# Kernel tuning notes

Hardware: AMD Instinct MI355X
Metric: run time of the kernel (lower is better)

## Reference

```python
import jax, jax.numpy as jnp
import numpy as np

B, T, DIM = 2, 2048, 1024
N_HEADS, HEAD_DIM, WINDOW = 16, 64, 512
EPS = 0.01


def _rmsnorm(x, gamma, eps):
    # x: [B, T, H*D] float32; normalize over last dim
    rms = jnp.sqrt(jnp.mean(jnp.square(x), axis=-1, keepdims=True) + eps)
    return x / rms * gamma


def setup_inputs() -> dict:
    key = jax.random.key(0)
    ks = jax.random.split(key, 5)
    s = 1.0 / np.sqrt(DIM)
    return {
        "x": jax.random.normal(ks[0], (B, T, DIM), jnp.float32),
        "wq": jax.random.normal(ks[1], (N_HEADS * HEAD_DIM, DIM), jnp.float32) * s,
        "wk": jax.random.normal(ks[2], (N_HEADS * HEAD_DIM, DIM), jnp.float32) * s,
        "wv": jax.random.normal(ks[3], (N_HEADS * HEAD_DIM, DIM), jnp.float32) * s,
        "wo": jax.random.normal(ks[4], (DIM, N_HEADS * HEAD_DIM), jnp.float32) * s,
        "q_gamma": jnp.ones((N_HEADS * HEAD_DIM,), jnp.float32),
        "k_gamma": jnp.ones((N_HEADS * HEAD_DIM,), jnp.float32),
    }


def reference(x, wq, wk, wv, wo, q_gamma, k_gamma):
    Bx, Tx, _ = x.shape
    H, D = N_HEADS, HEAD_DIM
    # projections (Linear with weight [out,in]): [B,T,H*D]
    q = x @ wq.T
    k = x @ wk.T
    v = (x @ wv.T).reshape(Bx, Tx, H, D).transpose(0, 2, 1, 3)  # [B,H,T,D]
    # QK RMSNorm over the flattened H*D dimension (float32 math)
    q = _rmsnorm(q, q_gamma, 1e-6).reshape(Bx, Tx, H, D).transpose(0, 2, 1, 3)
    k = _rmsnorm(k, k_gamma, 1e-6).reshape(Bx, Tx, H, D).transpose(0, 2, 1, 3)
    scale = 1.0 / np.sqrt(D)
    scores = jnp.einsum("bhqd,bhkd->bhqk", q, k) * scale  # [B,H,T,T]
    # ALiBi bias: slopes[h] * (j - i)
    slopes = jnp.asarray([2.0 ** (-8.0 / H * (h + 1)) for h in range(H)], jnp.float32)
    pos = jnp.arange(Tx)
    dist = (pos[None, :] - pos[:, None]).astype(jnp.float32)  # [T,T], dist[i,j]=j-i
    scores = scores + slopes[None, :, None, None] * dist[None, None]
    # causal (j>i) OR beyond sliding window (i-j > window_size)
    j_minus_i = pos[None, :] - pos[:, None]
    mask = (j_minus_i > 0) | (j_minus_i < -WINDOW)
    scores = jnp.where(mask[None, None], -1e9, scores)
    attn = jax.nn.softmax(scores, axis=-1)
    out = jnp.einsum("bhqk,bhkd->bhqd", attn, v)  # [B,H,T,D]
    out = out.transpose(0, 2, 1, 3).reshape(Bx, Tx, H * D)
    return out @ wo.T
```

## Files before the change

kernel.cpp:

```cpp
#include <hip/hip_runtime.h>
#include <stdint.h>

typedef unsigned short u16;
typedef __bf16 bf16x8 __attribute__((ext_vector_type(8)));
typedef float f32x4 __attribute__((ext_vector_type(4)));

#define MFMA16(a, b, c) __builtin_amdgcn_mfma_f32_16x16x32_bf16((a), (b), (c), 0, 0, 0)

__device__ __forceinline__ u16 f2bf(float f) {
  union { float f; uint32_t u; } v; v.f = f;
  uint32_t r = v.u + 0x7fffu + ((v.u >> 16) & 1u);
  return (u16)(r >> 16);
}
__device__ __forceinline__ float bf2f(u16 h) {
  union { uint32_t u; float f; } v; v.u = ((uint32_t)h) << 16;
  return v.f;
}
__device__ __forceinline__ void gload_lds16(const void* g, void* l) {
  __builtin_amdgcn_global_load_lds(
      (const __attribute__((address_space(1))) uint32_t*)(uintptr_t)g,
      (__attribute__((address_space(3))) uint32_t*)(uintptr_t)l, 16, 0, 0);
}
__device__ __forceinline__ uint32_t cvt_pk_bf16(float a, float b) {
  uint32_t r;
  asm("v_cvt_pk_bf16_f32 %0, %1, %2" : "=v"(r) : "v"(a), "v"(b));
  return r;
}

__global__ void k_cvt_all(const float* __restrict__ x, const float* __restrict__ wq,
                          const float* __restrict__ wk, const float* __restrict__ wv,
                          const float* __restrict__ wo, u16* __restrict__ xb,
                          u16* __restrict__ wqb, u16* __restrict__ wkb, u16* __restrict__ wvb,
                          u16* __restrict__ wob) {
  const int i = blockIdx.x * 256 + threadIdx.x;
  const float* src; u16* dst; int off;
  if (i < 1048576)      { src = x;  dst = xb;  off = i; }
  else if (i < 1310720) { src = wq; dst = wqb; off = i - 1048576; }
  else if (i < 1572864) { src = wk; dst = wkb; off = i - 1310720; }
  else if (i < 1835008) { src = wv; dst = wvb; off = i - 1572864; }
  else                  { src = wo; dst = wob; off = i - 1835008; }
  const float4 v = ((const float4*)src)[off];
  u16 o[4] = { f2bf(v.x), f2bf(v.y), f2bf(v.z), f2bf(v.w) };
  *(uint2*)(dst + 4 * (size_t)off) = *(const uint2*)o;
}

template <bool BF16_OUT>
__device__ __forceinline__ void gemm_core(const u16* __restrict__ A, const u16* __restrict__ Bw,
                                          void* __restrict__ C) {
  constexpr int K = 1024, N = 1024;
  __shared__ __align__(16) u16 As[128 * 32];
  __shared__ __align__(16) u16 Bs[128 * 32];
  const int tid = threadIdx.x, l = tid & 63, w = tid >> 6;
  const int wm = (w >> 1) * 64, wn = (w & 1) * 64;
  const int tn = blockIdx.x * 128, tm = blockIdx.y * 128;
  const int lo = l & 15, hi8 = (l >> 4) * 8;
  f32x4 acc[4][4] = {};

  const int srow = l >> 2, scol = (l & 3) * 8;
  for (int kt = 0; kt < K; kt += 32) {
    __syncthreads();
#pragma unroll
    for (int j = 0; j < 2; ++j) {
      const int c = w * 2 + j;
      const int row = c * 16 + srow;
      gload_lds16(A + (size_t)(tm + row) * K + kt + scol, &As[c * 512]);
      gload_lds16(Bw + (size_t)(tn + row) * K + kt + scol, &Bs[c * 512]);
    }
    __syncthreads();
    bf16x8 af[4], bfr[4];
#pragma unroll
    for (int m = 0; m < 4; ++m) af[m] = *(const bf16x8*)&As[(wm + m * 16 + lo) * 32 + hi8];
#pragma unroll
    for (int n = 0; n < 4; ++n) bfr[n] = *(const bf16x8*)&Bs[(wn + n * 16 + lo) * 32 + hi8];
#pragma unroll
    for (int m = 0; m < 4; ++m)
#pragma unroll
      for (int n = 0; n < 4; ++n) acc[m][n] = MFMA16(af[m], bfr[n], acc[m][n]);
  }
  const int r0 = (l >> 4) * 4;
#pragma unroll
  for (int m = 0; m < 4; ++m)
#pragma unroll
    for (int n = 0; n < 4; ++n)
#pragma unroll
      for (int r = 0; r < 4; ++r) {
        const size_t idx = (size_t)(tm + wm + m * 16 + r0 + r) * N + (tn + wn + n * 16 + lo);
        if (BF16_OUT) ((u16*)C)[idx] = f2bf(acc[m][n][r]);
        else ((float*)C)[idx] = acc[m][n][r];
      }
}

__global__ __launch_bounds__(256, 2) void k_gemm_qkv(
    const u16* __restrict__ X, const u16* __restrict__ Wq, const u16* __restrict__ Wk,
    const u16* __restrict__ Wv, u16* __restrict__ Q, u16* __restrict__ Kt, u16* __restrict__ V) {
  const u16* B = blockIdx.z == 0 ? Wq : blockIdx.z == 1 ? Wk : Wv;
  u16* C = blockIdx.z == 0 ? Q : blockIdx.z == 1 ? Kt : V;
  gemm_core<true>(X, B, C);
}
__global__ __launch_bounds__(256, 2) void k_gemm_out(const u16* __restrict__ Ao,
                                                     const u16* __restrict__ Wo,
                                                     float* __restrict__ C) {
  gemm_core<false>(Ao, Wo, C);
}

__global__ __launch_bounds__(256) void k_rmsnorm(u16* __restrict__ Q, u16* __restrict__ Kt,
                                                 const float* __restrict__ qg,
                                                 const float* __restrict__ kg) {
  const int row = blockIdx.x;
  u16* base = (row < 4096) ? (Q + (size_t)row * 1024) : (Kt + (size_t)(row - 4096) * 1024);
  const float* g = (row < 4096) ? qg : kg;
  const int tid = threadIdx.x;
  ushort4 v = ((const ushort4*)base)[tid];
  float f0 = bf2f(v.x), f1 = bf2f(v.y), f2 = bf2f(v.z), f3 = bf2f(v.w);
  float ss = f0 * f0 + f1 * f1 + f2 * f2 + f3 * f3;
#pragma unroll
  for (int off = 32; off >= 1; off >>= 1) ss += __shfl_xor(ss, off, 64);
  __shared__ float wsum[4];
  if ((tid & 63) == 0) wsum[tid >> 6] = ss;
  __syncthreads();
  ss = wsum[0] + wsum[1] + wsum[2] + wsum[3];
  const float rinv = rsqrtf(ss * (1.0f / 1024.0f) + 1e-6f);
  const float4 gv = ((const float4*)g)[tid];
  v.x = f2bf(f0 * rinv * gv.x);
  v.y = f2bf(f1 * rinv * gv.y);
  v.z = f2bf(f2 * rinv * gv.z);
  v.w = f2bf(f3 * rinv * gv.w);
  ((ushort4*)base)[tid] = v;
}

__global__ __launch_bounds__(512, 4) void k_attn(const u16* __restrict__ Q,
                                                 const u16* __restrict__ Kt,
                                                 const u16* __restrict__ V,
                                                 u16* __restrict__ O) {
  constexpr int T = 2048, HD = 1024, WIN = 512;
  const int qb = blockIdx.x * 128, h = blockIdx.y, b = blockIdx.z;
  const int tid = threadIdx.x, l = tid & 63, w = tid >> 6;
  const int lo = l & 15, hi = l >> 4;
  const int qw = qb + w * 16;
  const int qg = qw + lo;

  __shared__ __align__(16) u16 Ks[2][64 * 64];
  __shared__ __align__(16) u16 Vt[2][64 * 72];

  const size_t bT = (size_t)b * T;

  bf16x8 qf[2];
  {
    const u16* Qr = Q + (bT + qw + lo) * HD + h * 64 + hi * 8;
    qf[0] = *(const bf16x8*)(Qr);
    qf[1] = *(const bf16x8*)(Qr + 32);
  }

  const int srow = tid >> 3;
  const int kcol = 8 * ((tid & 7) ^ (srow & 7));
  const int vkv = 2 * (l & 31) + (l >> 5);
  const int vd0 = w * 8;
  const u16* Kg0 = Kt + bT * HD + h * 64;
  const u16* Vg0 = V + bT * HD + h * 64;

  float m_r = -1e30f, l_r = 0.f;
  f32x4 o_acc[4] = {};

  const float L2E = 1.4426950408889634f;
  const float scaleL = 0.125f * L2E;
  const float slopeL = exp2f(-0.5f * (float)(h + 1)) * L2E;
  float cn[4], cr[4];
#pragma unroll
  for (int n = 0; n < 4; ++n) cn[n] = slopeL * (float)(n * 16);
#pragma unroll
  for (int r = 0; r < 4; ++r) cr[r] = slopeL * (float)r;

  const int kvs = (qb >= WIN) ? (qb - WIN) : 0;
  const int nt = (qb + 128 - kvs) >> 6;

  gload_lds16(Kg0 + (size_t)(kvs + srow) * HD + kcol, &Ks[0][tid * 8]);
  {
    const uint4 pkt = *(const uint4*)(Vg0 + (size_t)(kvs + vkv) * HD + vd0);
    const u16* e = (const u16*)&pkt;
#pragma unroll
    for (int j = 0; j < 8; ++j) Vt[0][(vd0 + j) * 72 + vkv] = e[j];
  }
  __syncthreads();

  for (int t = 0; t < nt; ++t) {
    const int kv0 = kvs + t * 64, cur = t & 1;
    const bool pf_next = (t + 1 < nt);
    uint4 vnext;
    if (pf_next) {
      gload_lds16(Kg0 + (size_t)(kv0 + 64 + srow) * HD + kcol, &Ks[cur ^ 1][tid * 8]);
      vnext = *(const uint4*)(Vg0 + (size_t)(kv0 + 64 + vkv) * HD + vd0);
    }

    const bool active = (kv0 <= qw + 15) && (kv0 + 63 + WIN >= qw);
    if (active) {
      f32x4 st[4];
      __builtin_amdgcn_s_setprio(1);
#pragma unroll
      for (int n = 0; n < 4; ++n) {
        f32x4 z = {0.f, 0.f, 0.f, 0.f};
        const int row = n * 16 + lo;
        const int swz = (row & 7) << 4;
#pragma unroll
        for (int kk = 0; kk < 2; ++kk) {
          const bf16x8 kf =
              *(const bf16x8*)((const char*)Ks[cur] + row * 128 + ((kk * 64 + hi * 16) ^ swz));
          z = MFMA16(kf, qf[kk], z);
        }
        st[n] = z;
      }
      __builtin_amdgcn_s_setprio(0);

      const int ddb = kv0 + hi * 4 - qg;
      const float bb = slopeL * (float)ddb;
      float bn[4];
#pragma unroll
      for (int n = 0; n < 4; ++n) bn[n] = bb + cn[n];
      const bool interior = (kv0 + 63 <= qw) && (qw + 15 - kv0 <= WIN);
      if (interior) {
#pragma unroll
        for (int n = 0; n < 4; ++n)
#pragma unroll
          for (int r = 0; r < 4; ++r) st[n][r] = st[n][r] * scaleL + (bn[n] + cr[r]);
      } else {
#pragma unroll
        for (int n = 0; n < 4; ++n)
#pragma unroll
          for (int r = 0; r < 4; ++r) {
            const int dd = ddb + n * 16 + r;
            const float s_ = st[n][r] * scaleL + (bn[n] + cr[r]);
            st[n][r] = (dd > 0 || dd < -WIN) ? -1e30f : s_;
          }
      }

      float mx = -1e30f;
#pragma unroll
      for (int n = 0; n < 4; ++n) {
        const float a = fmaxf(st[n][0], st[n][1]), c = fmaxf(st[n][2], st[n][3]);
        mx = fmaxf(mx, fmaxf(a, c));
      }
      mx = fmaxf(mx, __shfl_xor(mx, 16, 64));
      mx = fmaxf(mx, __shfl_xor(mx, 32, 64));
      const float mn = fmaxf(m_r, mx);
      const float alpha = exp2f(m_r - mn);
      m_r = mn;

      float rs = 0.f;
#pragma unroll
      for (int n = 0; n < 4; ++n)
#pragma unroll
        for (int r = 0; r < 4; ++r) {
          const float p = exp2f(st[n][r] - mn);
          st[n][r] = p;
          rs += p;
        }
      rs += __shfl_xor(rs, 16, 64);
      rs += __shfl_xor(rs, 32, 64);
      l_r = l_r * alpha + rs;
#pragma unroll
      for (int nd = 0; nd < 4; ++nd)
#pragma unroll
        for (int r = 0; r < 4; ++r) o_acc[nd][r] *= alpha;

      uint32_t pk[4][2];
#pragma unroll
      for (int n = 0; n < 4; ++n)
#pragma unroll
        for (int d = 0; d < 2; ++d) pk[n][d] = cvt_pk_bf16(st[n][2 * d], st[n][2 * d + 1]);

      uint32_t pfr[2][4];
#pragma unroll
      for (int kk = 0; kk < 2; ++kk)
#pragma unroll
        for (int d = 0; d < 2; ++d) {
          auto s1 = __builtin_amdgcn_permlane32_swap(pk[kk * 2][d], pk[kk * 2 + 1][d], false, false);
          auto s2 = __builtin_amdgcn_permlane16_swap(s1[0], s1[1], false, false);
          pfr[kk][d] = s2[0];
          pfr[kk][2 + d] = s2[1];
        }

      __builtin_amdgcn_s_setprio(1);
#pragma unroll
      for (int kk = 0; kk < 2; ++kk) {
        union { uint32_t u[4]; bf16x8 v; } pu;
#pragma unroll
        for (int d2 = 0; d2 < 4; ++d2) pu.u[d2] = pfr[kk][d2];
        const bf16x8 pv = pu.v;
#pragma unroll
        for (int nd = 0; nd < 4; ++nd) {
          const bf16x8 vf = *(const bf16x8*)&Vt[cur][(nd * 16 + lo) * 72 + kk * 32 + hi * 8];
          o_acc[nd] = MFMA16(vf, pv, o_acc[nd]);
        }
      }
      __builtin_amdgcn_s_setprio(0);
    }

    if (pf_next) {
      const u16* e = (const u16*)&vnext;
#pragma unroll
      for (int j = 0; j < 8; ++j) Vt[cur ^ 1][(vd0 + j) * 72 + vkv] = e[j];
    }
    __syncthreads();
  }

  const float inv = 1.f / l_r;
  u16* Og = O + (bT + qw + lo) * HD + h * 64;
#pragma unroll
  for (int nd = 0; nd < 4; ++nd) {
    uint2 pack;
    pack.x = cvt_pk_bf16(o_acc[nd][0] * inv, o_acc[nd][1] * inv);
    pack.y = cvt_pk_bf16(o_acc[nd][2] * inv, o_acc[nd][3] * inv);
    *(uint2*)(Og + nd * 16 + hi * 4) = pack;
  }
}

extern "C" void kernel_launch(void* const* d_in, const int* in_sizes, int n_in,
                              void* d_out, int out_size, void* d_ws, size_t ws_size,
                              hipStream_t stream) {
  const float* x = (const float*)d_in[0];
  const float* wq = (const float*)d_in[1];
  const float* wk = (const float*)d_in[2];
  const float* wv = (const float*)d_in[3];
  const float* wo = (const float*)d_in[4];
  const float* qg = (const float*)d_in[5];
  const float* kg = (const float*)d_in[6];
  float* out = (float*)d_out;

  char* ws = (char*)d_ws;
  const size_t MB = (size_t)1 << 20;
  u16* xb  = (u16*)(ws + 0 * MB);
  u16* wqb = (u16*)(ws + 8 * MB);
  u16* wkb = (u16*)(ws + 10 * MB);
  u16* wvb = (u16*)(ws + 12 * MB);
  u16* wob = (u16*)(ws + 14 * MB);
  u16* qb  = (u16*)(ws + 16 * MB);
  u16* kb  = (u16*)(ws + 24 * MB);
  u16* vb  = (u16*)(ws + 32 * MB);
  u16* ab  = xb;

  k_cvt_all<<<8192, 256, 0, stream>>>(x, wq, wk, wv, wo, xb, wqb, wkb, wvb, wob);
  k_gemm_qkv<<<dim3(8, 32, 3), 256, 0, stream>>>(xb, wqb, wkb, wvb, qb, kb, vb);
  k_rmsnorm<<<8192, 256, 0, stream>>>(qb, kb, qg, kg);
  k_attn<<<dim3(16, 16, 2), 512, 0, stream>>>(qb, kb, vb, ab);
  k_gemm_out<<<dim3(8, 32, 1), 256, 0, stream>>>(ab, wob, out);
}
```

Before: 109.8 us.

## Double-buffer GEMM LDS staging and remap attention blocks with manual waitcnt barriers

The GEMM core now keeps two LDS buffers and issues global-to-LDS loads two k-tiles ahead, replacing the paired __syncthreads with explicit vmcnt waits and raw barriers so memory loads overlap MFMA work. The GEMM kernels' occupancy hint moves from 2 to 3 blocks per CU. The attention kernel remaps its linear block index so neighbouring blocks are spread across query tiles, heads and batch, which should balance the uneven sliding-window work. It also replaces __syncthreads with hand-placed waitcnt and barrier instructions. Hand-counted vmcnt values are fragile: a wrong count could read stale LDS, and the larger LDS footprint may limit residency.

Measured after the change: 106.3 us. 3.2% less time.

```diff
diff --git a/kernel.cpp b/kernel.cpp
--- a/kernel.cpp
+++ b/kernel.cpp
@@ -47,9 +47,9 @@
 template <bool BF16_OUT>
 __device__ __forceinline__ void gemm_core(const u16* __restrict__ A, const u16* __restrict__ Bw,
                                           void* __restrict__ C) {
-  constexpr int K = 1024, N = 1024;
-  __shared__ __align__(16) u16 As[128 * 32];
-  __shared__ __align__(16) u16 Bs[128 * 32];
+  constexpr int K = 1024, N = 1024, NT = K / 32;
+  __shared__ __align__(16) u16 As[2][128 * 32];
+  __shared__ __align__(16) u16 Bs[2][128 * 32];
   const int tid = threadIdx.x, l = tid & 63, w = tid >> 6;
   const int wm = (w >> 1) * 64, wn = (w & 1) * 64;
   const int tn = blockIdx.x * 128, tm = blockIdx.y * 128;
@@ -57,26 +57,51 @@
   f32x4 acc[4][4] = {};
 
   const int srow = l >> 2, scol = (l & 3) * 8;
-  for (int kt = 0; kt < K; kt += 32) {
-    __syncthreads();
-#pragma unroll
-    for (int j = 0; j < 2; ++j) {
-      const int c = w * 2 + j;
-      const int row = c * 16 + srow;
-      gload_lds16(A + (size_t)(tm + row) * K + kt + scol, &As[c * 512]);
-      gload_lds16(Bw + (size_t)(tn + row) * K + kt + scol, &Bs[c * 512]);
+  const int c0 = w * 2, c1 = w * 2 + 1;
+  const u16* Ag0 = A + (size_t)(tm + c0 * 16 + srow) * K + scol;
+  const u16* Ag1 = A + (size_t)(tm + c1 * 16 + srow) * K + scol;
+  const u16* Bg0 = Bw + (size_t)(tn + c0 * 16 + srow) * K + scol;
+  const u16* Bg1 = Bw + (size_t)(tn + c1 * 16 + srow) * K + scol;
+
+#define STAGE_G(t, buf)                           \
+  {                                               \
+    const int kt_ = (t) * 32;                     \
+    gload_lds16(Ag0 + kt_, &As[(buf)][c0 * 512]); \
+    gload_lds16(Ag1 + kt_, &As[(buf)][c1 * 512]); \
+    gload_lds16(Bg0 + kt_, &Bs[(buf)][c0 * 512]); \
+    gload_lds16(Bg1 + kt_, &Bs[(buf)][c1 * 512]); \
+  }
+
+  STAGE_G(0, 0);
+  STAGE_G(1, 1);
+
+  for (int t = 0; t < NT; ++t) {
+    const int cur = t & 1;
+    if (t + 1 < NT) {
+      asm volatile("s_waitcnt vmcnt(4)");
+    } else {
+      asm volatile("s_waitcnt vmcnt(0)");
     }
-    __syncthreads();
+    __builtin_amdgcn_s_barrier();
+    __builtin_amdgcn_sched_barrier(0);
+
     bf16x8 af[4], bfr[4];
 #pragma unroll
-    for (int m = 0; m < 4; ++m) af[m] = *(const bf16x8*)&As[(wm + m * 16 + lo) * 32 + hi8];
-#pragma unroll
-    for (int n = 0; n < 4; ++n) bfr[n] = *(const bf16x8*)&Bs[(wn + n * 16 + lo) * 32 + hi8];
+    for (int m = 0; m < 4; ++m) af[m] = *(const bf16x8*)&As[cur][(wm + m * 16 + lo) * 32 + hi8];
+#pragma unroll
+    for (int n = 0; n < 4; ++n) bfr[n] = *(const bf16x8*)&Bs[cur][(wn + n * 16 + lo) * 32 + hi8];
 #pragma unroll
     for (int m = 0; m < 4; ++m)
 #pragma unroll
       for (int n = 0; n < 4; ++n) acc[m][n] = MFMA16(af[m], bfr[n], acc[m][n]);
-  }
+
+    __builtin_amdgcn_sched_barrier(0);
+    __builtin_amdgcn_s_barrier();
+    __builtin_amdgcn_sched_barrier(0);
+    if (t + 2 < NT) STAGE_G(t + 2, cur);
+  }
+#undef STAGE_G
+
   const int r0 = (l >> 4) * 4;
 #pragma unroll
   for (int m = 0; m < 4; ++m)
@@ -90,14 +115,14 @@
       }
 }
 
-__global__ __launch_bounds__(256, 2) void k_gemm_qkv(
+__global__ __launch_bounds__(256, 3) void k_gemm_qkv(
     const u16* __restrict__ X, const u16* __restrict__ Wq, const u16* __restrict__ Wk,
     const u16* __restrict__ Wv, u16* __restrict__ Q, u16* __restrict__ Kt, u16* __restrict__ V) {
   const u16* B = blockIdx.z == 0 ? Wq : blockIdx.z == 1 ? Wk : Wv;
   u16* C = blockIdx.z == 0 ? Q : blockIdx.z == 1 ? Kt : V;
   gemm_core<true>(X, B, C);
 }
-__global__ __launch_bounds__(256, 2) void k_gemm_out(const u16* __restrict__ Ao,
+__global__ __launch_bounds__(256, 3) void k_gemm_out(const u16* __restrict__ Ao,
                                                      const u16* __restrict__ Wo,
                                                      float* __restrict__ C) {
   gemm_core<false>(Ao, Wo, C);
@@ -133,7 +158,9 @@
                                                  const u16* __restrict__ V,
                                                  u16* __restrict__ O) {
   constexpr int T = 2048, HD = 1024, WIN = 512;
-  const int qb = blockIdx.x * 128, h = blockIdx.y, b = blockIdx.z;
+  const int nlin = blockIdx.x + (blockIdx.y << 4) + (blockIdx.z << 8);
+  const int wid = (nlin & 7) * 64 + (nlin >> 3);
+  const int qb = (wid & 15) * 128, h = (wid >> 4) & 15, b = wid >> 8;
   const int tid = threadIdx.x, l = tid & 63, w = tid >> 6;
   const int lo = l & 15, hi = l >> 4;
   const int qw = qb + w * 16;
@@ -173,23 +200,31 @@
   const int kvs = (qb >= WIN) ? (qb - WIN) : 0;
   const int nt = (qb + 128 - kvs) >> 6;
 
-  gload_lds16(Kg0 + (size_t)(kvs + srow) * HD + kcol, &Ks[0][tid * 8]);
   {
     const uint4 pkt = *(const uint4*)(Vg0 + (size_t)(kvs + vkv) * HD + vd0);
+    gload_lds16(Kg0 + (size_t)(kvs + srow) * HD + kcol, &Ks[0][tid * 8]);
     const u16* e = (const u16*)&pkt;
 #pragma unroll
     for (int j = 0; j < 8; ++j) Vt[0][(vd0 + j) * 72 + vkv] = e[j];
   }
-  __syncthreads();
+  asm volatile("s_waitcnt vmcnt(0)");
+  asm volatile("s_waitcnt lgkmcnt(0)");
+  __builtin_amdgcn_s_barrier();
+  __builtin_amdgcn_sched_barrier(0);
 
   for (int t = 0; t < nt; ++t) {
     const int kv0 = kvs + t * 64, cur = t & 1;
     const bool pf_next = (t + 1 < nt);
     uint4 vnext;
     if (pf_next) {
+      vnext = *(const uint4*)(Vg0 + (size_t)(kv0 + 64 + vkv) * HD + vd0);
       gload_lds16(Kg0 + (size_t)(kv0 + 64 + srow) * HD + kcol, &Ks[cur ^ 1][tid * 8]);
-      vnext = *(const uint4*)(Vg0 + (size_t)(kv0 + 64 + vkv) * HD + vd0);
+      asm volatile("s_waitcnt vmcnt(2)");
+    } else {
+      asm volatile("s_waitcnt vmcnt(0)");
     }
+    __builtin_amdgcn_s_barrier();
+    __builtin_amdgcn_sched_barrier(0);
 
     const bool active = (kv0 <= qw + 15) && (kv0 + 63 + WIN >= qw);
     if (active) {
@@ -299,7 +334,10 @@
 #pragma unroll
       for (int j = 0; j < 8; ++j) Vt[cur ^ 1][(vd0 + j) * 72 + vkv] = e[j];
     }
-    __syncthreads();
+    __builtin_amdgcn_sched_barrier(0);
+    asm volatile("s_waitcnt lgkmcnt(0)");
+    __builtin_amdgcn_s_barrier();
+    __builtin_amdgcn_sched_barrier(0);
   }
 
   const float inv = 1.f / l_r;
```
